# Kernel optimization log

Hardware: AMD Instinct MI355X
Metric: run time of the kernel (lower is better)

## Reference

```python
import jax, jax.numpy as jnp
import numpy as np

B, CIN, H, W = 32, 64, 128, 128
HID, OUT, E, S, R = 64, 64, 8, 2, 16
TOP_K = 2
TEMP = 2.0
BN_EPS = 1e-5


def setup_inputs() -> dict:
    key = jax.random.key(0)
    ks = jax.random.split(key, 16)
    sc = lambda fan: 1.0 / np.sqrt(fan)
    h2 = 2 * HID
    return {
        "x": jax.random.normal(ks[0], (B, CIN, H, W), jnp.float32),
        "fe_w": jax.random.normal(ks[1], (HID, CIN), jnp.float32) * sc(CIN),
        "fe_b": jnp.zeros((HID,), jnp.float32),
        "s_w": jax.random.normal(ks[2], (S, OUT, HID), jnp.float32) * sc(HID),
        "s_b": jnp.zeros((S, OUT), jnp.float32),
        "e_w": jax.random.normal(ks[3], (E, OUT, HID), jnp.float32) * sc(HID),
        "e_b": jnp.zeros((E, OUT), jnp.float32),
        "g1_w": jax.random.normal(ks[4], (h2, HID), jnp.float32) * sc(HID),
        "g1_b": jnp.zeros((h2,), jnp.float32),
        "bn1_g": jnp.ones((h2,), jnp.float32),
        "bn1_b": jnp.zeros((h2,), jnp.float32),
        "ca1_w": jax.random.normal(ks[5], (h2 // R, h2), jnp.float32) * sc(h2),
        "ca1_b": jnp.zeros((h2 // R,), jnp.float32),
        "ca2_w": jax.random.normal(ks[6], (h2, h2 // R), jnp.float32) * sc(h2 // R),
        "ca2_b": jnp.zeros((h2,), jnp.float32),
        "g2_w": jax.random.normal(ks[7], (HID, h2), jnp.float32) * sc(h2),
        "g2_b": jnp.zeros((HID,), jnp.float32),
        "bn2_g": jnp.ones((HID,), jnp.float32),
        "bn2_b": jnp.zeros((HID,), jnp.float32),
        "g3_w": jax.random.normal(ks[8], (E, HID), jnp.float32) * sc(HID),
        "g3_b": jnp.zeros((E,), jnp.float32),
    }


def _gelu(v):
    return jax.nn.gelu(v, approximate=False)


def _bn_eval(v, g, b):
    # BatchNorm eval mode with running_mean=0, running_var=1
    return v * (g / np.sqrt(1.0 + BN_EPS)) + b


def reference(x, fe_w, fe_b, s_w, s_b, e_w, e_b, g1_w, g1_b, bn1_g, bn1_b,
              ca1_w, ca1_b, ca2_w, ca2_b, g2_w, g2_b, bn2_g, bn2_b, g3_w, g3_b):
    # feature extractor: 1x1 conv + GELU
    features = _gelu(jnp.einsum('bchw,oc->bohw', x, fe_w) + fe_b[None, :, None, None])

    # shared experts: mean of S expert outputs (sum / S)
    shared = _gelu(jnp.einsum('bchw,soc->bsohw', features, s_w)
                   + s_b[None, :, :, None, None]).mean(axis=1)

    # gating on globally pooled features [B, HID]
    gf = features.mean(axis=(2, 3))
    h1 = _gelu(_bn_eval(gf @ g1_w.T + g1_b, bn1_g, bn1_b))  # [B, 2*HID]
    # ChannelAttention on 1x1 spatial: avg_pool == max_pool == identity
    att = _gelu(h1 @ ca1_w.T + ca1_b) @ ca2_w.T + ca2_b
    h1 = h1 * jax.nn.sigmoid(att + att)  # avg_out + max_out are identical
    hh = _gelu(_bn_eval(h1 @ g2_w.T + g2_b, bn2_g, bn2_b))  # [B, HID]
    scores = hh @ g3_w.T + g3_b  # [B, E]

    top_vals, top_idx = jax.lax.top_k(scores, TOP_K)
    top_w = jax.nn.softmax(top_vals / TEMP, axis=1)  # [B, TOP_K]
    # dense per-(sample, expert) weights
    dense_w = jnp.zeros((x.shape[0], E), scores.dtype).at[
        jnp.arange(x.shape[0])[:, None], top_idx].add(top_w)

    # all experts on full batch, then weighted accumulate (matches original loop)
    eo = _gelu(jnp.einsum('bchw,eoc->beohw', features, e_w)
               + e_b[None, :, :, None, None])  # [B, E, OUT, H, W]
    routed = jnp.einsum('beohw,be->bohw', eo, dense_w)

    return shared + routed
```

## Files before the change

kernel.cpp:

```cpp
#include <hip/hip_runtime.h>
#include <hip/hip_bf16.h>
#include <stdint.h>

#define HW 16384

typedef __bf16 bf16_t;
typedef bf16_t bf16x8 __attribute__((ext_vector_type(8)));
typedef float f32x4 __attribute__((ext_vector_type(4)));

__device__ __forceinline__ float gelu_f(float x) {
    float t = x * fmaf(x * x, 0.044715f, 1.0f);
    float e = __builtin_amdgcn_exp2f(-2.3022083f * t);
    return x * __builtin_amdgcn_rcpf(1.0f + e);
}

__device__ __forceinline__ uint32_t pk2(float a, float b) {
    union { bf16_t h[2]; uint32_t u; } z;
    z.h[0] = (bf16_t)a; z.h[1] = (bf16_t)b;
    return z.u;
}

__device__ __forceinline__ void load16_to_lds(const float* g, float* lds) {
    __builtin_amdgcn_global_load_lds(
        (const __attribute__((address_space(1))) uint32_t*)g,
        (__attribute__((address_space(3))) uint32_t*)lds, 16, 0, 0);
}

__device__ __forceinline__ bf16x8 frag8(const float* src) {
    float4 lo = ((const float4*)src)[0];
    float4 hi = ((const float4*)src)[1];
    bf16x8 r;
    r[0] = (bf16_t)lo.x; r[1] = (bf16_t)lo.y; r[2] = (bf16_t)lo.z; r[3] = (bf16_t)lo.w;
    r[4] = (bf16_t)hi.x; r[5] = (bf16_t)hi.y; r[6] = (bf16_t)hi.z; r[7] = (bf16_t)hi.w;
    return r;
}

__device__ __forceinline__ bf16x8 frag44(const float* a, const float* b) {
    float4 lo = *(const float4*)a;
    float4 hi = *(const float4*)b;
    bf16x8 r;
    r[0] = (bf16_t)lo.x; r[1] = (bf16_t)lo.y; r[2] = (bf16_t)lo.z; r[3] = (bf16_t)lo.w;
    r[4] = (bf16_t)hi.x; r[5] = (bf16_t)hi.y; r[6] = (bf16_t)hi.z; r[7] = (bf16_t)hi.w;
    return r;
}

__global__ __launch_bounds__(256, 4)
void k1_feat(const float* __restrict__ x, const float* __restrict__ fe_w,
             const float* __restrict__ fe_b, bf16_t* __restrict__ feat,
             float* __restrict__ gf_part) {
    __shared__ float xs[4][32 * 64];
    __shared__ float gf4[4][64];

    int tid = threadIdx.x;
    int lane = tid & 63;
    int wid = tid >> 6;
    int r16 = lane & 15;
    int g = lane >> 4;
    int gtile = blockIdx.x * 4 + wid;
    int b = gtile >> 9;
    int p0 = (gtile & 511) * 32;

    bf16x8 A[4][2];
    f32x4 bias[4];
#pragma unroll
    for (int ot = 0; ot < 4; ++ot) {
#pragma unroll
        for (int kh = 0; kh < 2; ++kh)
            A[ot][kh] = frag8(fe_w + (ot * 16 + r16) * 64 + kh * 32 + g * 8);
#pragma unroll
        for (int r = 0; r < 4; ++r) bias[ot][r] = fe_b[ot * 16 + g * 4 + r];
    }
    asm volatile("" ::: "memory");

    float* xw = &xs[wid][0];
    {
        int rl = lane >> 3;
        int ch0 = lane & 7;
#pragma unroll
        for (int s = 0; s < 8; ++s) {
            int row = s * 8 + rl;
            int gch = ch0 ^ ((s & 3) << 1);
            const float* gsrc = x + (size_t)(b * 64 + row) * HW + p0 + gch * 4;
            load16_to_lds(gsrc, xw + s * 256);
        }
    }

    int cm0 = ((((r16 >> 2) + 0) ^ (g << 1)) << 2) + (r16 & 3);
    int cm1 = ((((r16 >> 2) + 4) ^ (g << 1)) << 2) + (r16 & 3);

    float gfp[4][4] = {};
    bf16_t* featb = feat + (size_t)b * HW * 64;

    asm volatile("s_waitcnt vmcnt(4)" ::: "memory");

    f32x4 y0[4], y1[4];
    {
        bf16x8 B00, B10;
#pragma unroll
        for (int j = 0; j < 8; ++j) {
            int ro = (g * 8 + j) * 32;
            B00[j] = (bf16_t)xw[ro + cm0];
            B10[j] = (bf16_t)xw[ro + cm1];
        }
#pragma unroll
        for (int ot = 0; ot < 4; ++ot) {
            f32x4 z = {0.f, 0.f, 0.f, 0.f};
            y0[ot] = __builtin_amdgcn_mfma_f32_16x16x32_bf16(A[ot][0], B00, z, 0, 0, 0);
            y1[ot] = __builtin_amdgcn_mfma_f32_16x16x32_bf16(A[ot][0], B10, z, 0, 0, 0);
        }
    }
    asm volatile("s_waitcnt vmcnt(0)" ::: "memory");
    {
        bf16x8 B01, B11;
#pragma unroll
        for (int j = 0; j < 8; ++j) {
            int ro = (32 + g * 8 + j) * 32;
            B01[j] = (bf16_t)xw[ro + cm0];
            B11[j] = (bf16_t)xw[ro + cm1];
        }
#pragma unroll
        for (int ot = 0; ot < 4; ++ot) {
            y0[ot] = __builtin_amdgcn_mfma_f32_16x16x32_bf16(A[ot][1], B01, y0[ot], 0, 0, 0);
            y1[ot] = __builtin_amdgcn_mfma_f32_16x16x32_bf16(A[ot][1], B11, y1[ot], 0, 0, 0);
        }
    }

#pragma unroll
    for (int a = 0; a < 2; ++a) {
        f32x4* y = a ? y1 : y0;
        float vals[4][4];
#pragma unroll
        for (int ot = 0; ot < 4; ++ot)
#pragma unroll
            for (int r = 0; r < 4; ++r) {
                float v = gelu_f(y[ot][r] + bias[ot][r]);
                gfp[ot][r] += v;
                vals[ot][r] = v;
            }
        uint4 lo, hi;
        lo.x = pk2(vals[0][0], vals[0][1]); lo.y = pk2(vals[0][2], vals[0][3]);
        lo.z = pk2(vals[1][0], vals[1][1]); lo.w = pk2(vals[1][2], vals[1][3]);
        hi.x = pk2(vals[2][0], vals[2][1]); hi.y = pk2(vals[2][2], vals[2][3]);
        hi.z = pk2(vals[3][0], vals[3][1]); hi.w = pk2(vals[3][2], vals[3][3]);
        int px = p0 + a * 16 + r16;
        uint4* dst = (uint4*)(featb + (size_t)px * 64 + g * 16);
        dst[0] = lo;
        dst[1] = hi;
    }

#pragma unroll
    for (int ot = 0; ot < 4; ++ot)
#pragma unroll
        for (int r = 0; r < 4; ++r) {
            float v = gfp[ot][r];
            v += __shfl_xor(v, 1);
            v += __shfl_xor(v, 2);
            v += __shfl_xor(v, 4);
            v += __shfl_xor(v, 8);
            if (r16 == 0) gf4[wid][ot * 16 + g * 4 + r] = v;
        }
    __syncthreads();
    if (tid < 64)
        gf_part[(size_t)blockIdx.x * 64 + tid] =
            gf4[0][tid] + gf4[1][tid] + gf4[2][tid] + gf4[3][tid];
}

__global__ __launch_bounds__(256)
void k2_gate(const float* __restrict__ gf_part,
             const float* __restrict__ g1_w, const float* __restrict__ g1_b,
             const float* __restrict__ bn1_g, const float* __restrict__ bn1_b,
             const float* __restrict__ ca1_w, const float* __restrict__ ca1_b,
             const float* __restrict__ ca2_w, const float* __restrict__ ca2_b,
             const float* __restrict__ g2_w, const float* __restrict__ g2_b,
             const float* __restrict__ bn2_g, const float* __restrict__ bn2_b,
             const float* __restrict__ g3_w, const float* __restrict__ g3_b,
             int* __restrict__ gidx, float* __restrict__ gw) {
    __shared__ float w1t[128 * 65];
    __shared__ float wc1[8 * 129];
    __shared__ float wc2[128 * 9];
    __shared__ float w2t[64 * 129];
    __shared__ float w3[8 * 65];
    __shared__ float gf[64], h1[128], a1[8], hh[64], sc[8];
    const float R1 = 0.99999500003749969f;
    int tid = threadIdx.x;
    int b = blockIdx.x;

    for (int i = tid; i < 2048; i += 256) {
        float4 v = ((const float4*)g1_w)[i];
        float* d = w1t + (i >> 4) * 65 + (i & 15) * 4;
        d[0] = v.x; d[1] = v.y; d[2] = v.z; d[3] = v.w;
    }
    for (int i = tid; i < 2048; i += 256) {
        float4 v = ((const float4*)g2_w)[i];
        float* d = w2t + (i >> 5) * 129 + (i & 31) * 4;
        d[0] = v.x; d[1] = v.y; d[2] = v.z; d[3] = v.w;
    }
    if (tid < 256) {
        int i = tid;
        float4 v = ((const float4*)ca1_w)[i];
        float* d = wc1 + (i >> 5) * 129 + (i & 31) * 4;
        d[0] = v.x; d[1] = v.y; d[2] = v.z; d[3] = v.w;
    }
    if (tid < 256) {
        int i = tid;
        float4 v = ((const float4*)ca2_w)[i];
        float* d = wc2 + (i >> 1) * 9 + (i & 1) * 4;
        d[0] = v.x; d[1] = v.y; d[2] = v.z; d[3] = v.w;
    }
    if (tid < 128) {
        int i = tid;
        float4 v = ((const float4*)g3_w)[i];
        float* d = w3 + (i >> 4) * 65 + (i & 15) * 4;
        d[0] = v.x; d[1] = v.y; d[2] = v.z; d[3] = v.w;
    }
    if (tid < 64) {
        float s0 = 0.f, s1 = 0.f, s2 = 0.f, s3 = 0.f;
        const float* gp = gf_part + (size_t)b * 128 * 64 + tid;
#pragma unroll 8
        for (int i = 0; i < 128; i += 4) {
            s0 += gp[(size_t)(i + 0) * 64];
            s1 += gp[(size_t)(i + 1) * 64];
            s2 += gp[(size_t)(i + 2) * 64];
            s3 += gp[(size_t)(i + 3) * 64];
        }
        gf[tid] = ((s0 + s1) + (s2 + s3)) * (1.0f / 16384.0f);
    }
    __syncthreads();

    if (tid < 128) {
        int j = tid;
        float s0 = 0.f, s1 = 0.f;
#pragma unroll 8
        for (int c = 0; c < 64; c += 2) {
            s0 += gf[c] * w1t[j * 65 + c];
            s1 += gf[c + 1] * w1t[j * 65 + c + 1];
        }
        float s = g1_b[j] + s0 + s1;
        s = s * (bn1_g[j] * R1) + bn1_b[j];
        h1[j] = gelu_f(s);
    }
    __syncthreads();
    if (tid < 8) {
        int j = tid;
        float s0 = 0.f, s1 = 0.f;
#pragma unroll 8
        for (int c = 0; c < 128; c += 2) {
            s0 += h1[c] * wc1[j * 129 + c];
            s1 += h1[c + 1] * wc1[j * 129 + c + 1];
        }
        a1[j] = gelu_f(ca1_b[j] + s0 + s1);
    }
    __syncthreads();
    if (tid < 128) {
        int j = tid;
        float s = ca2_b[j];
#pragma unroll
        for (int r = 0; r < 8; ++r) s += a1[r] * wc2[j * 9 + r];
        float e2 = __builtin_amdgcn_exp2f(-2.8853901f * s);
        h1[j] = h1[j] * __builtin_amdgcn_rcpf(1.0f + e2);
    }
    __syncthreads();
    if (tid < 64) {
        int j = tid;
        float s0 = 0.f, s1 = 0.f;
#pragma unroll 8
        for (int c = 0; c < 128; c += 2) {
            s0 += h1[c] * w2t[j * 129 + c];
            s1 += h1[c + 1] * w2t[j * 129 + c + 1];
        }
        float s = g2_b[j] + s0 + s1;
        s = s * (bn2_g[j] * R1) + bn2_b[j];
        hh[j] = gelu_f(s);
    }
    __syncthreads();
    if (tid < 8) {
        int j = tid;
        float s0 = 0.f, s1 = 0.f;
#pragma unroll 8
        for (int c = 0; c < 64; c += 2) {
            s0 += hh[c] * w3[j * 65 + c];
            s1 += hh[c + 1] * w3[j * 65 + c + 1];
        }
        sc[j] = g3_b[j] + s0 + s1;
    }
    __syncthreads();
    if (tid == 0) {
        float v0 = -1e30f, v1 = -1e30f;
        int i0 = 0, i1 = 0;
#pragma unroll
        for (int e = 0; e < 8; ++e) {
            float s = sc[e];
            if (s > v0) { v1 = v0; i1 = i0; v0 = s; i0 = e; }
            else if (s > v1) { v1 = s; i1 = e; }
        }
        float t = __builtin_amdgcn_exp2f(0.7213475f * (v1 - v0));
        float den = __builtin_amdgcn_rcpf(1.0f + t);
        gidx[b * 2] = i0; gidx[b * 2 + 1] = i1;
        gw[b * 2] = den; gw[b * 2 + 1] = t * den;
    }
}

__global__ __launch_bounds__(256, 4)
void k3_out(const bf16_t* __restrict__ feat, const float* __restrict__ s_w,
            const float* __restrict__ s_b, const float* __restrict__ e_w,
            const float* __restrict__ e_b, const int* __restrict__ gidx,
            const float* __restrict__ gw, float* __restrict__ out) {
    int tid = threadIdx.x;
    int lane = tid & 63, wid = tid >> 6;
    int r16 = lane & 15, g = lane >> 4;
    int b = blockIdx.x >> 6;
    int stripe = blockIdx.x & 63;

    int i0 = gidx[2 * b], i1 = gidx[2 * b + 1];
    float coef[4] = {0.5f, 0.5f, gw[2 * b], gw[2 * b + 1]};
    const float* Wm[4] = {s_w, s_w + 4096,
                          e_w + (size_t)i0 * 4096, e_w + (size_t)i1 * 4096};
    const float* Bv[4] = {s_b, s_b + 64, e_b + i0 * 64, e_b + i1 * 64};

    bf16x8 Wf[4][2];
    float bias[4];
    int row = wid * 16 + r16;
#pragma unroll
    for (int m = 0; m < 4; ++m) {
#pragma unroll
        for (int kh = 0; kh < 2; ++kh) {
            int base = (g & 1) * 32 + (kh * 2 + (g >> 1)) * 4;
            Wf[m][kh] = frag44(Wm[m] + row * 64 + base,
                               Wm[m] + row * 64 + base + 16);
        }
        bias[m] = Bv[m][row];
    }

    const uint4* fb = (const uint4*)(feat + (size_t)b * HW * 64);
    float* outb = out + ((size_t)b * 64 + row) * HW + stripe * 256;
    int pbase = stripe * 256 + r16;

    auto BODY = [&](int t, uint4 u0, uint4 u1) {
        bf16x8 F0 = __builtin_bit_cast(bf16x8, u0);
        bf16x8 F1 = __builtin_bit_cast(bf16x8, u1);
        f32x4 acc = {0.f, 0.f, 0.f, 0.f};
#pragma unroll
        for (int m = 0; m < 4; ++m) {
            f32x4 y = {0.f, 0.f, 0.f, 0.f};
            y = __builtin_amdgcn_mfma_f32_16x16x32_bf16(F0, Wf[m][0], y, 0, 0, 0);
            y = __builtin_amdgcn_mfma_f32_16x16x32_bf16(F1, Wf[m][1], y, 0, 0, 0);
#pragma unroll
            for (int r = 0; r < 4; ++r)
                acc[r] += coef[m] * gelu_f(y[r] + bias[m]);
        }
        float4 st = {acc[0], acc[1], acc[2], acc[3]};
        *(float4*)(outb + t * 16 + g * 4) = st;
    };

    uint4 a0 = fb[(size_t)pbase * 8 + g];
    uint4 a1 = fb[(size_t)pbase * 8 + 4 + g];
    uint4 b0 = fb[(size_t)(pbase + 16) * 8 + g];
    uint4 b1 = fb[(size_t)(pbase + 16) * 8 + 4 + g];
#pragma unroll
    for (int t = 0; t < 14; t += 2) {
        uint4 n0 = fb[(size_t)(pbase + (t + 2) * 16) * 8 + g];
        uint4 n1 = fb[(size_t)(pbase + (t + 2) * 16) * 8 + 4 + g];
        BODY(t, a0, a1); a0 = n0; a1 = n1;
        uint4 m0 = fb[(size_t)(pbase + (t + 3) * 16) * 8 + g];
        uint4 m1 = fb[(size_t)(pbase + (t + 3) * 16) * 8 + 4 + g];
        BODY(t + 1, b0, b1); b0 = m0; b1 = m1;
    }
    BODY(14, a0, a1);
    BODY(15, b0, b1);
}

extern "C" void kernel_launch(void* const* d_in, const int* in_sizes, int n_in,
                              void* d_out, int out_size, void* d_ws, size_t ws_size,
                              hipStream_t stream) {
    (void)in_sizes; (void)n_in; (void)out_size; (void)ws_size;
    const float* x     = (const float*)d_in[0];
    const float* fe_w  = (const float*)d_in[1];
    const float* fe_b  = (const float*)d_in[2];
    const float* s_w   = (const float*)d_in[3];
    const float* s_b   = (const float*)d_in[4];
    const float* e_w   = (const float*)d_in[5];
    const float* e_b   = (const float*)d_in[6];
    const float* g1_w  = (const float*)d_in[7];
    const float* g1_b  = (const float*)d_in[8];
    const float* bn1_g = (const float*)d_in[9];
    const float* bn1_b = (const float*)d_in[10];
    const float* ca1_w = (const float*)d_in[11];
    const float* ca1_b = (const float*)d_in[12];
    const float* ca2_w = (const float*)d_in[13];
    const float* ca2_b = (const float*)d_in[14];
    const float* g2_w  = (const float*)d_in[15];
    const float* g2_b  = (const float*)d_in[16];
    const float* bn2_g = (const float*)d_in[17];
    const float* bn2_b = (const float*)d_in[18];
    const float* g3_w  = (const float*)d_in[19];
    const float* g3_b  = (const float*)d_in[20];
    float* out = (float*)d_out;

    char* wsb = (char*)d_ws;
    bf16_t* feat   = (bf16_t*)wsb;
    float* gf_part = (float*)(wsb + 67108864);
    int* gidx      = (int*)(wsb + 67108864 + 1048576);
    float* gwts    = (float*)(wsb + 67108864 + 1048576 + 256);

    k1_feat<<<4096, 256, 0, stream>>>(x, fe_w, fe_b, feat, gf_part);
    k2_gate<<<32, 256, 0, stream>>>(gf_part, g1_w, g1_b, bn1_g, bn1_b, ca1_w, ca1_b,
                                    ca2_w, ca2_b, g2_w, g2_b, bn2_g, bn2_b, g3_w, g3_b,
                                    gidx, gwts);
    k3_out<<<2048, 256, 0, stream>>>(feat, s_w, s_b, e_w, e_b, gidx, gwts, out);
}
```

Before: 343.0 us.

## Double-buffer x tiles in k1_feat and process four tiles per wave

Each wave now handles four consecutive 32-pixel tiles instead of one. The x loads go into a double-buffered LDS region so that global-to-LDS copies for the next tile overlap the MFMA and GELU work on the current one. The grid shrinks from 4096 to 1024 blocks, and the gate kernel's partial-sum reduction is adjusted to the smaller number of partials. In exchange, LDS use per block doubles and launch bounds drop to 2 blocks per CU, which may lower occupancy, and the hand-written vmcnt wait counts have to match the load ordering exactly.

```diff
diff --git a/kernel.cpp b/kernel.cpp
--- a/kernel.cpp
+++ b/kernel.cpp
@@ -44,11 +44,13 @@
     return r;
 }
 
-__global__ __launch_bounds__(256, 4)
+#define PIN asm volatile("" ::: "memory")
+
+__global__ __launch_bounds__(256, 2)
 void k1_feat(const float* __restrict__ x, const float* __restrict__ fe_w,
              const float* __restrict__ fe_b, bf16_t* __restrict__ feat,
              float* __restrict__ gf_part) {
-    __shared__ float xs[4][32 * 64];
+    __shared__ float xs[4][2][32 * 64];
     __shared__ float gf4[4][64];
 
     int tid = threadIdx.x;
@@ -56,9 +58,9 @@
     int wid = tid >> 6;
     int r16 = lane & 15;
     int g = lane >> 4;
-    int gtile = blockIdx.x * 4 + wid;
-    int b = gtile >> 9;
-    int p0 = (gtile & 511) * 32;
+    int gtile0 = blockIdx.x * 16 + wid * 4;
+    int b = gtile0 >> 9;
+    int px0 = (gtile0 & 511) * 32;
 
     bf16x8 A[4][2];
     f32x4 bias[4];
@@ -67,23 +69,23 @@
 #pragma unroll
         for (int kh = 0; kh < 2; ++kh)
             A[ot][kh] = frag8(fe_w + (ot * 16 + r16) * 64 + kh * 32 + g * 8);
-#pragma unroll
-        for (int r = 0; r < 4; ++r) bias[ot][r] = fe_b[ot * 16 + g * 4 + r];
-    }
-    asm volatile("" ::: "memory");
-
-    float* xw = &xs[wid][0];
-    {
-        int rl = lane >> 3;
-        int ch0 = lane & 7;
+        bias[ot] = *(const f32x4*)(fe_b + ot * 16 + g * 4);
+    }
+    PIN;
+
+    float* xw = &xs[wid][0][0];
+    int rl = lane >> 3;
+    int ch0 = lane & 7;
+
+    auto STAGE = [&](int buf, int t) {
 #pragma unroll
         for (int s = 0; s < 8; ++s) {
             int row = s * 8 + rl;
             int gch = ch0 ^ ((s & 3) << 1);
-            const float* gsrc = x + (size_t)(b * 64 + row) * HW + p0 + gch * 4;
-            load16_to_lds(gsrc, xw + s * 256);
-        }
-    }
+            const float* gsrc = x + (size_t)(b * 64 + row) * HW + px0 + t * 32 + gch * 4;
+            load16_to_lds(gsrc, xw + buf * 2048 + s * 256);
+        }
+    };
 
     int cm0 = ((((r16 >> 2) + 0) ^ (g << 1)) << 2) + (r16 & 3);
     int cm1 = ((((r16 >> 2) + 4) ^ (g << 1)) << 2) + (r16 & 3);
@@ -91,62 +93,70 @@
     float gfp[4][4] = {};
     bf16_t* featb = feat + (size_t)b * HW * 64;
 
-    asm volatile("s_waitcnt vmcnt(4)" ::: "memory");
-
-    f32x4 y0[4], y1[4];
-    {
-        bf16x8 B00, B10;
+    auto COMPUTE = [&](int buf, int t) {
+        const float* xb = xw + buf * 2048;
+        bf16x8 B00, B10, B01, B11;
 #pragma unroll
         for (int j = 0; j < 8; ++j) {
-            int ro = (g * 8 + j) * 32;
-            B00[j] = (bf16_t)xw[ro + cm0];
-            B10[j] = (bf16_t)xw[ro + cm1];
-        }
+            int ro0 = (g * 8 + j) * 32;
+            int ro1 = (32 + g * 8 + j) * 32;
+            B00[j] = (bf16_t)xb[ro0 + cm0];
+            B10[j] = (bf16_t)xb[ro0 + cm1];
+            B01[j] = (bf16_t)xb[ro1 + cm0];
+            B11[j] = (bf16_t)xb[ro1 + cm1];
+        }
+        f32x4 y0[4], y1[4];
 #pragma unroll
         for (int ot = 0; ot < 4; ++ot) {
             f32x4 z = {0.f, 0.f, 0.f, 0.f};
-            y0[ot] = __builtin_amdgcn_mfma_f32_16x16x32_bf16(A[ot][0], B00, z, 0, 0, 0);
-            y1[ot] = __builtin_amdgcn_mfma_f32_16x16x32_bf16(A[ot][0], B10, z, 0, 0, 0);
-        }
-    }
-    asm volatile("s_waitcnt vmcnt(0)" ::: "memory");
-    {
-        bf16x8 B01, B11;
-#pragma unroll
-        for (int j = 0; j < 8; ++j) {
-            int ro = (32 + g * 8 + j) * 32;
-            B01[j] = (bf16_t)xw[ro + cm0];
-            B11[j] = (bf16_t)xw[ro + cm1];
-        }
-#pragma unroll
-        for (int ot = 0; ot < 4; ++ot) {
-            y0[ot] = __builtin_amdgcn_mfma_f32_16x16x32_bf16(A[ot][1], B01, y0[ot], 0, 0, 0);
-            y1[ot] = __builtin_amdgcn_mfma_f32_16x16x32_bf16(A[ot][1], B11, y1[ot], 0, 0, 0);
-        }
-    }
-
-#pragma unroll
-    for (int a = 0; a < 2; ++a) {
-        f32x4* y = a ? y1 : y0;
-        float vals[4][4];
-#pragma unroll
-        for (int ot = 0; ot < 4; ++ot)
-#pragma unroll
-            for (int r = 0; r < 4; ++r) {
-                float v = gelu_f(y[ot][r] + bias[ot][r]);
-                gfp[ot][r] += v;
-                vals[ot][r] = v;
-            }
-        uint4 lo, hi;
-        lo.x = pk2(vals[0][0], vals[0][1]); lo.y = pk2(vals[0][2], vals[0][3]);
-        lo.z = pk2(vals[1][0], vals[1][1]); lo.w = pk2(vals[1][2], vals[1][3]);
-        hi.x = pk2(vals[2][0], vals[2][1]); hi.y = pk2(vals[2][2], vals[2][3]);
-        hi.z = pk2(vals[3][0], vals[3][1]); hi.w = pk2(vals[3][2], vals[3][3]);
-        int px = p0 + a * 16 + r16;
-        uint4* dst = (uint4*)(featb + (size_t)px * 64 + g * 16);
-        dst[0] = lo;
-        dst[1] = hi;
-    }
+            z = __builtin_amdgcn_mfma_f32_16x16x32_bf16(A[ot][0], B00, z, 0, 0, 0);
+            y0[ot] = __builtin_amdgcn_mfma_f32_16x16x32_bf16(A[ot][1], B01, z, 0, 0, 0);
+            f32x4 w = {0.f, 0.f, 0.f, 0.f};
+            w = __builtin_amdgcn_mfma_f32_16x16x32_bf16(A[ot][0], B10, w, 0, 0, 0);
+            y1[ot] = __builtin_amdgcn_mfma_f32_16x16x32_bf16(A[ot][1], B11, w, 0, 0, 0);
+        }
+#pragma unroll
+        for (int a = 0; a < 2; ++a) {
+            f32x4* y = a ? y1 : y0;
+            float vals[4][4];
+#pragma unroll
+            for (int ot = 0; ot < 4; ++ot)
+#pragma unroll
+                for (int r = 0; r < 4; ++r) {
+                    float v = gelu_f(y[ot][r] + bias[ot][r]);
+                    gfp[ot][r] += v;
+                    vals[ot][r] = v;
+                }
+            uint4 lo, hi;
+            lo.x = pk2(vals[0][0], vals[0][1]); lo.y = pk2(vals[0][2], vals[0][3]);
+            lo.z = pk2(vals[1][0], vals[1][1]); lo.w = pk2(vals[1][2], vals[1][3]);
+            hi.x = pk2(vals[2][0], vals[2][1]); hi.y = pk2(vals[2][2], vals[2][3]);
+            hi.z = pk2(vals[3][0], vals[3][1]); hi.w = pk2(vals[3][2], vals[3][3]);
+            int px = px0 + t * 32 + a * 16 + r16;
+            uint4* dst = (uint4*)(featb + (size_t)px * 64 + g * 16);
+            dst[0] = lo;
+            dst[1] = hi;
+        }
+    };
+
+    STAGE(0, 0);
+    STAGE(1, 1);
+    PIN;
+    asm volatile("s_waitcnt vmcnt(8)" ::: "memory");
+    COMPUTE(0, 0);
+    PIN;
+    STAGE(0, 2);
+    PIN;
+    asm volatile("s_waitcnt vmcnt(12)" ::: "memory");
+    COMPUTE(1, 1);
+    PIN;
+    STAGE(1, 3);
+    PIN;
+    asm volatile("s_waitcnt vmcnt(12)" ::: "memory");
+    COMPUTE(0, 2);
+    PIN;
+    asm volatile("s_waitcnt vmcnt(4)" ::: "memory");
+    COMPUTE(1, 3);
 
 #pragma unroll
     for (int ot = 0; ot < 4; ++ot)
@@ -214,16 +224,14 @@
         d[0] = v.x; d[1] = v.y; d[2] = v.z; d[3] = v.w;
     }
     if (tid < 64) {
-        float s0 = 0.f, s1 = 0.f, s2 = 0.f, s3 = 0.f;
-        const float* gp = gf_part + (size_t)b * 128 * 64 + tid;
+        float s0 = 0.f, s1 = 0.f;
+        const float* gp = gf_part + (size_t)b * 32 * 64 + tid;
 #pragma unroll 8
-        for (int i = 0; i < 128; i += 4) {
+        for (int i = 0; i < 32; i += 2) {
             s0 += gp[(size_t)(i + 0) * 64];
             s1 += gp[(size_t)(i + 1) * 64];
-            s2 += gp[(size_t)(i + 2) * 64];
-            s3 += gp[(size_t)(i + 3) * 64];
-        }
-        gf[tid] = ((s0 + s1) + (s2 + s3)) * (1.0f / 16384.0f);
+        }
+        gf[tid] = (s0 + s1) * (1.0f / 16384.0f);
     }
     __syncthreads();
 
@@ -402,7 +410,7 @@
     int* gidx      = (int*)(wsb + 67108864 + 1048576);
     float* gwts    = (float*)(wsb + 67108864 + 1048576 + 256);
 
-    k1_feat<<<4096, 256, 0, stream>>>(x, fe_w, fe_b, feat, gf_part);
+    k1_feat<<<1024, 256, 0, stream>>>(x, fe_w, fe_b, feat, gf_part);
     k2_gate<<<32, 256, 0, stream>>>(gf_part, g1_w, g1_b, bn1_g, bn1_b, ca1_w, ca1_b,
                                     ca2_w, ca2_b, g2_w, g2_b, bn2_g, bn2_b, g3_w, g3_b,
                                     gidx, gwts);
```

Measured after the change: 342.2 us. Within noise of the previous version (-0.2%).
